# Optimization experiments

Hardware: AMD Instinct MI355X
Metric: run time of the kernel (lower is better)

## Reference

```python
import jax, jax.numpy as jnp
import numpy as np

N, D_IN, D_H, D_OUT, R, E, NB = 50000, 128, 128, 64, 4, 400000, 2

def _xavier(k, shape, fan_in, fan_out):
    # torch xavier_uniform with relu gain sqrt(2)
    lim = np.sqrt(2.0) * np.sqrt(6.0 / (fan_in + fan_out))
    return jax.random.uniform(k, shape, jnp.float32, -lim, lim)

def setup_inputs() -> dict:
    key = jax.random.key(0)
    ks = jax.random.split(key, 9)
    x = jax.random.normal(ks[0], (N, D_IN), dtype=jnp.float32)
    src = jax.random.randint(ks[1], (R, E), 0, N, dtype=jnp.int32)
    dst = jax.random.randint(ks[2], (R, E), 0, N, dtype=jnp.int32)
    inp = {"x": x, "src": src, "dst": dst}
    dims = [(D_IN, D_H), (D_H, D_H), (D_H, D_OUT)]
    for i, (di, do) in enumerate(dims):
        inp[f"basis{i}"] = _xavier(ks[3 + 2 * i], (NB, di, do), di, do)
        inp[f"coeff{i}"] = _xavier(ks[4 + 2 * i], (R, NB), NB, R)
    return inp

def _rel_layer(h, src, dst, basis, coeff):
    """One RelGraphConvLayer: per-relation basis weight + GraphConv(norm='both'),
    summed over relations (HeteroGraphConv aggregate='sum')."""
    n = h.shape[0]
    W = jnp.einsum('rb,bio->rio', coeff, basis)  # [R, d_in, d_out] basis-decomposed weights
    out = jnp.zeros((n, W.shape[-1]), dtype=h.dtype)
    for r in range(src.shape[0]):  # fixed small set of relations
        s, d = src[r], dst[r]
        ones = jnp.ones(s.shape[0], dtype=h.dtype)
        deg_out = jnp.maximum(jax.ops.segment_sum(ones, s, num_segments=n), 1.0)
        deg_in = jnp.maximum(jax.ops.segment_sum(ones, d, num_segments=n), 1.0)
        norm_src = deg_out ** -0.5
        norm_dst = deg_in ** -0.5
        # weight applied before aggregation (d_in >= d_out path of dgl GraphConv; math identical)
        hr = (h * norm_src[:, None]) @ W[r]            # [N, d_out]
        agg = jax.ops.segment_sum(hr[s], d, num_segments=n)  # SpMM via gather + scatter-add
        out = out + agg * norm_dst[:, None]
    return out

def reference(x, src, dst, basis0, coeff0, basis1, coeff1, basis2, coeff2):
    h = jax.nn.relu(_rel_layer(x, src, dst, basis0, coeff0))
    h = jax.nn.relu(_rel_layer(h, src, dst, basis1, coeff1))
    return _rel_layer(h, src, dst, basis2, coeff2)  # final layer: no activation
```

## Files before the change

kernel.cpp:

```cpp
#include <hip/hip_runtime.h>
#include <hip/hip_bf16.h>
#include <cstdint>
#include <cstddef>

#define NN 50000
#define RR 4
#define EE 400000
#define TE (RR*EE)
#define HR 25000
#define RN (RR*NN)
#define NSEG (NN*RR)
#define SCB2 782
#define NBK 512
#define BKSZ 98
#define CHA 4000
#define MAXSPAN 4608

using frag_ab = __attribute__((ext_vector_type(8))) short;
using frag_cd = __attribute__((ext_vector_type(4))) float;

static __device__ __forceinline__ unsigned short f2bf(float f) {
    union { float f; unsigned u; } v; v.f = f;
    unsigned r = (v.u + 0x7FFF + ((v.u >> 16) & 1)) >> 16;
    return (unsigned short)r;
}
static __device__ __forceinline__ unsigned pack2(float lo, float hi) {
    return (unsigned)f2bf(lo) | ((unsigned)f2bf(hi) << 16);
}
static __device__ __forceinline__ float blo(unsigned u) { return __uint_as_float(u << 16); }
static __device__ __forceinline__ float bhi(unsigned u) { return __uint_as_float(u & 0xFFFF0000u); }

__global__ __launch_bounds__(1024) void k_hist(const int* __restrict__ src,
                                               const int* __restrict__ dst,
                                               int* __restrict__ cnt_srcQ,
                                               int* __restrict__ cnt_dstQ) {
    __shared__ unsigned bins[HR / 2];
    int combo = blockIdx.x >> 3;
    int range = (blockIdx.x >> 2) & 1;
    int qc    = blockIdx.x & 3;
    int r = combo >> 1;
    int side = combo & 1;
    const int* arr = (side == 0 ? src : dst) + (size_t)r * EE + (size_t)qc * (EE / 4);
    int lo = range * HR;
    for (int i = threadIdx.x; i < HR / 2; i += 1024) bins[i] = 0;
    __syncthreads();
    const int4* a4 = (const int4*)arr;
    for (int i = threadIdx.x; i < EE / 16; i += 1024) {
        int4 v = a4[i];
        int t;
        t = v.x - lo; if ((unsigned)t < (unsigned)HR) atomicAdd(&bins[t >> 1], 1u << ((t & 1) * 16));
        t = v.y - lo; if ((unsigned)t < (unsigned)HR) atomicAdd(&bins[t >> 1], 1u << ((t & 1) * 16));
        t = v.z - lo; if ((unsigned)t < (unsigned)HR) atomicAdd(&bins[t >> 1], 1u << ((t & 1) * 16));
        t = v.w - lo; if ((unsigned)t < (unsigned)HR) atomicAdd(&bins[t >> 1], 1u << ((t & 1) * 16));
    }
    __syncthreads();
    int* outp = (side == 0 ? cnt_srcQ : cnt_dstQ) + (size_t)qc * RN + (size_t)r * NN + lo;
    for (int i = threadIdx.x; i < HR / 2; i += 1024) {
        unsigned b = bins[i];
        outp[2 * i]     = (int)(b & 0xFFFFu);
        outp[2 * i + 1] = (int)(b >> 16);
    }
}

__global__ __launch_bounds__(256) void k_sum_norms(const int* __restrict__ cnt_srcQ,
                                                   const int* __restrict__ cnt_dstQ,
                                                   float* __restrict__ nsrc,
                                                   float* __restrict__ ndst,
                                                   int* __restrict__ cntd2) {
    int i = blockIdx.x * 256 + threadIdx.x;
    if (i >= RN) return;
    int ss = cnt_srcQ[i] + cnt_srcQ[RN + i] + cnt_srcQ[2 * RN + i] + cnt_srcQ[3 * RN + i];
    int ds = cnt_dstQ[i] + cnt_dstQ[RN + i] + cnt_dstQ[2 * RN + i] + cnt_dstQ[3 * RN + i];
    nsrc[i] = 1.0f / sqrtf(fmaxf((float)ss, 1.0f));
    ndst[i] = 1.0f / sqrtf(fmaxf((float)ds, 1.0f));
    int r = i / NN, d = i - r * NN;
    cntd2[d * 4 + r] = ds;
}

__global__ __launch_bounds__(256) void k_partial(const int* __restrict__ cntd2,
                                                 int* __restrict__ part) {
    __shared__ int s[256];
    int t = threadIdx.x;
    int f = blockIdx.x * 256 + t;
    int v = (f < NSEG) ? cntd2[f] : 0;
    s[t] = v;
    __syncthreads();
    for (int off = 128; off > 0; off >>= 1) {
        if (t < off) s[t] += s[t + off];
        __syncthreads();
    }
    if (t == 0) part[blockIdx.x] = s[0];
}

__global__ __launch_bounds__(1024) void k_scan_small(const int* __restrict__ part,
                                                     int* __restrict__ offs) {
    __shared__ int s[1024];
    int t = threadIdx.x;
    s[t] = (t < SCB2) ? part[t] : 0;
    __syncthreads();
    for (int off = 1; off < 1024; off <<= 1) {
        int v = (t >= off) ? s[t - off] : 0;
        __syncthreads();
        s[t] += v;
        __syncthreads();
    }
    if (t < SCB2) offs[t] = (t == 0) ? 0 : s[t - 1];
}

__global__ __launch_bounds__(256) void k_emit(const int* __restrict__ cntd2,
                                              const int* __restrict__ offs,
                                              int* __restrict__ rp2,
                                              int* __restrict__ gcur) {
    __shared__ int s[256];
    int t = threadIdx.x;
    int f = blockIdx.x * 256 + t;
    int v = (f < NSEG) ? cntd2[f] : 0;
    s[t] = v;
    __syncthreads();
    for (int off = 1; off < 256; off <<= 1) {
        int u = (t >= off) ? s[t - off] : 0;
        __syncthreads();
        s[t] += u;
        __syncthreads();
    }
    if (f < NSEG) {
        int rv = offs[blockIdx.x] + s[t] - v;
        rp2[f] = rv;
        if (f % (BKSZ * 4) == 0) gcur[f / (BKSZ * 4)] = rv;
    }
    if (f == NSEG - 1) {
        rp2[NSEG] = TE;
        gcur[NBK - 1] = TE;
    }
}

__global__ __launch_bounds__(256) void k_fillA(const int* __restrict__ src,
                                               const int* __restrict__ dst,
                                               int* __restrict__ gcur,
                                               unsigned* __restrict__ stage) {
    __shared__ int cnt[NBK];
    __shared__ int rcur[NBK];
    int r = blockIdx.y;
    int base_e = blockIdx.x * CHA;
    int t = threadIdx.x;
    for (int i = t; i < NBK; i += 256) cnt[i] = 0;
    __syncthreads();
    const int* dr = dst + (size_t)r * EE;
    const int* sr = src + (size_t)r * EE;
    for (int i = base_e + t; i < base_e + CHA; i += 256) {
        int d = dr[i];
        atomicAdd(&cnt[d / BKSZ], 1);
    }
    __syncthreads();
    for (int i = t; i < NBK; i += 256) rcur[i] = atomicAdd(&gcur[i], cnt[i]);
    __syncthreads();
    for (int i = base_e + t; i < base_e + CHA; i += 256) {
        int d = dr[i];
        int s = sr[i];
        int b = d / BKSZ;
        int dl = d - b * BKSZ;
        int pos = atomicAdd(&rcur[b], 1);
        stage[pos] = (unsigned)s | ((unsigned)r << 16) | ((unsigned)dl << 18);
    }
}

__global__ __launch_bounds__(256) void k_fillB(const unsigned* __restrict__ stage,
                                               const int* __restrict__ rp2,
                                               const float* __restrict__ nsrc,
                                               const float* __restrict__ ndst,
                                               uint2* __restrict__ ed) {
    __shared__ unsigned imgU[MAXSPAN];
    __shared__ float imgW[MAXSPAN];
    __shared__ int lcur[BKSZ * 4];
    __shared__ float ndL[BKSZ * 4];
    int b = blockIdx.x;
    int t = threadIdx.x;
    int node0 = b * BKSZ;
    if (node0 >= NN) return;
    int nodes = min(BKSZ, NN - node0);
    int nseg_local = nodes * 4;
    int segbase = node0 * 4;
    for (int i = t; i < nseg_local; i += 256) {
        lcur[i] = rp2[segbase + i];
        ndL[i] = ndst[(i & 3) * NN + node0 + (i >> 2)];
    }
    __syncthreads();
    int S0 = rp2[segbase];
    int S1 = rp2[segbase + nseg_local];
    int span = S1 - S0;
    if (span <= MAXSPAN) {
        for (int i = S0 + t; i < S1; i += 256) {
            unsigned w = stage[i];
            int s = (int)(w & 0xFFFFu);
            int r = (int)((w >> 16) & 3u);
            int dl = (int)(w >> 18);
            int seg = dl * 4 + r;
            int pos = atomicAdd(&lcur[seg], 1);
            int idx = pos - S0;
            imgU[idx] = w & 0x3FFFFu;
            imgW[idx] = nsrc[r * NN + s] * ndL[seg];
        }
        __syncthreads();
        for (int i = t; i < span; i += 256)
            ed[S0 + i] = make_uint2(imgU[i], __float_as_uint(imgW[i]));
    } else {
        for (int i = S0 + t; i < S1; i += 256) {
            unsigned w = stage[i];
            int s = (int)(w & 0xFFFFu);
            int r = (int)((w >> 16) & 3u);
            int dl = (int)(w >> 18);
            int seg = dl * 4 + r;
            int pos = atomicAdd(&lcur[seg], 1);
            ed[pos] = make_uint2(w & 0x3FFFFu,
                                 __float_as_uint(nsrc[r * NN + s] * ndL[seg]));
        }
    }
}

__global__ __launch_bounds__(256) void k_cvt_all(const float4* __restrict__ x4,
                                                 uint2* __restrict__ o,
                                                 const float* __restrict__ B0,
                                                 const float* __restrict__ B1,
                                                 const float* __restrict__ B2,
                                                 unsigned short* __restrict__ Bt0,
                                                 unsigned short* __restrict__ Bt1,
                                                 unsigned short* __restrict__ Bt2) {
    int b = blockIdx.x;
    if (b < 6250) {
        int i = b * 256 + threadIdx.x;
        float4 v = x4[i];
        o[i] = make_uint2(pack2(v.x, v.y), pack2(v.z, v.w));
    } else {
        int t = (b - 6250) * 256 + threadIdx.x;
        if (t < 32768) {
            int k = t & 255, n = t >> 8;
            Bt0[t] = f2bf(B0[k * 128 + n]);
        } else if (t < 65536) {
            int i = t - 32768;
            int k = i & 255, n = i >> 8;
            Bt1[i] = f2bf(B1[k * 128 + n]);
        } else if (t < 81920) {
            int i = t - 65536;
            int k = i & 255, n = i >> 8;
            Bt2[i] = f2bf(B2[k * 64 + n]);
        }
    }
}

template <int BN, bool BF16OUT>
__global__ __launch_bounds__(512) void k_agg_gemm(const uint4* __restrict__ hb4,
                                                  const int* __restrict__ rp2,
                                                  const uint2* __restrict__ ed,
                                                  const float* __restrict__ coeff,
                                                  const unsigned short* __restrict__ Bt,
                                                  void* __restrict__ Cout) {
    __shared__ uint4 ldsA4[32 * 32];
    char* ldsB = (char*)ldsA4;

    int w = threadIdx.x >> 6;
    int lane = threadIdx.x & 63;
    int q = lane >> 4, hl = lane & 15;
    int node0 = blockIdx.x * 32;

    float c00 = coeff[0], c01 = coeff[1], c10 = coeff[2], c11 = coeff[3];
    float c20 = coeff[4], c21 = coeff[5], c30 = coeff[6], c31 = coeff[7];

#pragma unroll 1
    for (int k4 = 0; k4 < 4; k4++) {
        int rowl = w + k4 * 8;
        int node = node0 + rowl;
        if (node < NN) {
            float a00 = 0.f, a01 = 0.f, a02 = 0.f, a03 = 0.f;
            float a04 = 0.f, a05 = 0.f, a06 = 0.f, a07 = 0.f;
            float a10 = 0.f, a11 = 0.f, a12 = 0.f, a13 = 0.f;
            float a14 = 0.f, a15 = 0.f, a16 = 0.f, a17 = 0.f;

            int e0 = rp2[node * 4], e1 = rp2[node * 4 + 4];
            int e = e0;
            uint2 wA = make_uint2(0u, 0u), wB = make_uint2(0u, 0u);
            if (e + 7 < e1) { wA = ed[e + q]; wB = ed[e + 4 + q]; }
            for (; e + 7 < e1; e += 8) {
                uint4 hA = hb4[(size_t)(wA.x & 0xFFFFu) * 16 + hl];
                uint4 hB = hb4[(size_t)(wB.x & 0xFFFFu) * 16 + hl];
                int eN = (e + 15 < e1) ? (e + 8) : e0;
                uint2 nA = ed[eN + q];
                uint2 nB = ed[eN + 4 + q];

                int rA = (int)(wA.x >> 16);
                int rB = (int)(wB.x >> 16);
                float wsA = __uint_as_float(wA.y);
                float wsB = __uint_as_float(wB.y);
                float wa0 = (rA == 0 ? c00 : rA == 1 ? c10 : rA == 2 ? c20 : c30) * wsA;
                float wa1 = (rA == 0 ? c01 : rA == 1 ? c11 : rA == 2 ? c21 : c31) * wsA;
                float wb0 = (rB == 0 ? c00 : rB == 1 ? c10 : rB == 2 ? c20 : c30) * wsB;
                float wb1 = (rB == 0 ? c01 : rB == 1 ? c11 : rB == 2 ? c21 : c31) * wsB;

                float h0 = blo(hA.x), h1 = bhi(hA.x), h2 = blo(hA.y), h3 = bhi(hA.y);
                float h4 = blo(hA.z), h5 = bhi(hA.z), h6 = blo(hA.w), h7 = bhi(hA.w);
                a00 += wa0 * h0; a01 += wa0 * h1; a02 += wa0 * h2; a03 += wa0 * h3;
                a04 += wa0 * h4; a05 += wa0 * h5; a06 += wa0 * h6; a07 += wa0 * h7;
                a10 += wa1 * h0; a11 += wa1 * h1; a12 += wa1 * h2; a13 += wa1 * h3;
                a14 += wa1 * h4; a15 += wa1 * h5; a16 += wa1 * h6; a17 += wa1 * h7;

                h0 = blo(hB.x); h1 = bhi(hB.x); h2 = blo(hB.y); h3 = bhi(hB.y);
                h4 = blo(hB.z); h5 = bhi(hB.z); h6 = blo(hB.w); h7 = bhi(hB.w);
                a00 += wb0 * h0; a01 += wb0 * h1; a02 += wb0 * h2; a03 += wb0 * h3;
                a04 += wb0 * h4; a05 += wb0 * h5; a06 += wb0 * h6; a07 += wb0 * h7;
                a10 += wb1 * h0; a11 += wb1 * h1; a12 += wb1 * h2; a13 += wb1 * h3;
                a14 += wb1 * h4; a15 += wb1 * h5; a16 += wb1 * h6; a17 += wb1 * h7;

                wA = nA; wB = nB;
            }
            for (; e < e1; e += 4) {
                int E = e + q;
                bool act = E < e1;
                uint2 weA = ed[act ? E : e0];
                uint4 hA = hb4[(size_t)(weA.x & 0xFFFFu) * 16 + hl];
                int rA = (int)(weA.x >> 16);
                float wsA = act ? __uint_as_float(weA.y) : 0.f;
                float wa0 = (rA == 0 ? c00 : rA == 1 ? c10 : rA == 2 ? c20 : c30) * wsA;
                float wa1 = (rA == 0 ? c01 : rA == 1 ? c11 : rA == 2 ? c21 : c31) * wsA;
                float h0 = blo(hA.x), h1 = bhi(hA.x), h2 = blo(hA.y), h3 = bhi(hA.y);
                float h4 = blo(hA.z), h5 = bhi(hA.z), h6 = blo(hA.w), h7 = bhi(hA.w);
                a00 += wa0 * h0; a01 += wa0 * h1; a02 += wa0 * h2; a03 += wa0 * h3;
                a04 += wa0 * h4; a05 += wa0 * h5; a06 += wa0 * h6; a07 += wa0 * h7;
                a10 += wa1 * h0; a11 += wa1 * h1; a12 += wa1 * h2; a13 += wa1 * h3;
                a14 += wa1 * h4; a15 += wa1 * h5; a16 += wa1 * h6; a17 += wa1 * h7;
            }

            a00 += __shfl_xor(a00, 16, 64); a00 += __shfl_xor(a00, 32, 64);
            a01 += __shfl_xor(a01, 16, 64); a01 += __shfl_xor(a01, 32, 64);
            a02 += __shfl_xor(a02, 16, 64); a02 += __shfl_xor(a02, 32, 64);
            a03 += __shfl_xor(a03, 16, 64); a03 += __shfl_xor(a03, 32, 64);
            a04 += __shfl_xor(a04, 16, 64); a04 += __shfl_xor(a04, 32, 64);
            a05 += __shfl_xor(a05, 16, 64); a05 += __shfl_xor(a05, 32, 64);
            a06 += __shfl_xor(a06, 16, 64); a06 += __shfl_xor(a06, 32, 64);
            a07 += __shfl_xor(a07, 16, 64); a07 += __shfl_xor(a07, 32, 64);
            a10 += __shfl_xor(a10, 16, 64); a10 += __shfl_xor(a10, 32, 64);
            a11 += __shfl_xor(a11, 16, 64); a11 += __shfl_xor(a11, 32, 64);
            a12 += __shfl_xor(a12, 16, 64); a12 += __shfl_xor(a12, 32, 64);
            a13 += __shfl_xor(a13, 16, 64); a13 += __shfl_xor(a13, 32, 64);
            a14 += __shfl_xor(a14, 16, 64); a14 += __shfl_xor(a14, 32, 64);
            a15 += __shfl_xor(a15, 16, 64); a15 += __shfl_xor(a15, 32, 64);
            a16 += __shfl_xor(a16, 16, 64); a16 += __shfl_xor(a16, 32, 64);
            a17 += __shfl_xor(a17, 16, 64); a17 += __shfl_xor(a17, 32, 64);

            int c = q >> 1, h4 = q & 1;
            float v0 = c ? (h4 ? a14 : a10) : (h4 ? a04 : a00);
            float v1 = c ? (h4 ? a15 : a11) : (h4 ? a05 : a01);
            float v2 = c ? (h4 ? a16 : a12) : (h4 ? a06 : a02);
            float v3 = c ? (h4 ? a17 : a13) : (h4 ? a07 : a03);
            uint2 st;
            st.x = pack2(v0, v1);
            st.y = pack2(v2, v3);
            int idx8 = c * 32 + hl * 2 + h4;
            int boff = rowl * 512 + ((idx8 * 8) ^ ((rowl & 7) << 4));
            *(uint2*)(ldsB + boff) = st;
        }
    }
    __syncthreads();

    int strip = w & 1;
    int colgrp = w >> 1;
    int m = lane & 15, qq = lane >> 4;
    constexpr int NTW = BN / 64;

    frag_cd acc[NTW];
#pragma unroll
    for (int t = 0; t < NTW; t++) acc[t] = (frag_cd){0.f, 0.f, 0.f, 0.f};

    int arow = strip * 16 + m;
#pragma unroll
    for (int kc = 0; kc < 8; kc++) {
        int aoff = arow * 512 + ((qq * 16 + kc * 64) ^ ((arow & 7) << 4));
        frag_ab a = *(const frag_ab*)(ldsB + aoff);
#pragma unroll
        for (int t = 0; t < NTW; t++) {
            int ct = colgrp * NTW + t;
            frag_ab b = *(const frag_ab*)(Bt + (size_t)(ct * 16 + m) * 256 + kc * 32 + qq * 8);
            acc[t] = __builtin_amdgcn_mfma_f32_16x16x32_bf16(a, b, acc[t], 0, 0, 0);
        }
    }

    int row0 = node0 + strip * 16;
#pragma unroll
    for (int t = 0; t < NTW; t++) {
#pragma unroll
        for (int i = 0; i < 4; i++) {
            int row = row0 + qq * 4 + i;
            if (row < NN) {
                int col = (colgrp * NTW + t) * 16 + m;
                float v = acc[t][i];
                if (BF16OUT) {
                    v = fmaxf(v, 0.f);
                    ((unsigned short*)Cout)[(size_t)row * BN + col] = f2bf(v);
                } else {
                    ((float*)Cout)[(size_t)row * BN + col] = v;
                }
            }
        }
    }
}


extern "C" void kernel_launch(void* const* d_in, const int* in_sizes, int n_in,
                              void* d_out, int out_size, void* d_ws, size_t ws_size,
                              hipStream_t stream) {
    const float* x      = (const float*)d_in[0];
    const int*   src    = (const int*)d_in[1];
    const int*   dst    = (const int*)d_in[2];
    const float* basis0 = (const float*)d_in[3];
    const float* coeff0 = (const float*)d_in[4];
    const float* basis1 = (const float*)d_in[5];
    const float* coeff1 = (const float*)d_in[6];
    const float* basis2 = (const float*)d_in[7];
    const float* coeff2 = (const float*)d_in[8];
    float* out = (float*)d_out;

    char* p = (char*)d_ws;
    auto alloc = [&](size_t bytes) {
        char* r = p;
        p += (bytes + 255) & ~(size_t)255;
        return r;
    };
    int*   cnt_srcQ = (int*)alloc((size_t)4 * RN * 4);
    int*   cnt_dstQ = (int*)alloc((size_t)4 * RN * 4);
    float* nsrc     = (float*)alloc((size_t)RN * 4);
    float* ndst     = (float*)alloc((size_t)RN * 4);
    int*   cntd2    = (int*)alloc((size_t)NSEG * 4);
    int*   rp2      = (int*)alloc((size_t)(NSEG + 1) * 4);
    int*   part     = (int*)alloc((size_t)SCB2 * 4);
    int*   offs     = (int*)alloc((size_t)SCB2 * 4);
    int*   gcur     = (int*)alloc((size_t)NBK * 4);
    unsigned* stage = (unsigned*)alloc((size_t)TE * 4);
    uint2* ed       = (uint2*)alloc((size_t)TE * 8);
    unsigned* Hb    = (unsigned*)alloc((size_t)NN * 64 * 4);
    unsigned* Hb2   = (unsigned*)alloc((size_t)NN * 64 * 4);
    unsigned* Xb    = (unsigned*)alloc((size_t)NN * 64 * 4);
    unsigned short* Bt0 = (unsigned short*)alloc((size_t)128 * 256 * 2);
    unsigned short* Bt1 = (unsigned short*)alloc((size_t)128 * 256 * 2);
    unsigned short* Bt2 = (unsigned short*)alloc((size_t)64 * 256 * 2);

    k_cvt_all<<<6570, 256, 0, stream>>>((const float4*)x, (uint2*)Xb,
                                        basis0, basis1, basis2, Bt0, Bt1, Bt2);
    k_hist<<<64, 1024, 0, stream>>>(src, dst, cnt_srcQ, cnt_dstQ);
    k_sum_norms<<<(RN + 255) / 256, 256, 0, stream>>>(cnt_srcQ, cnt_dstQ, nsrc, ndst, cntd2);
    k_partial<<<SCB2, 256, 0, stream>>>(cntd2, part);
    k_scan_small<<<1, 1024, 0, stream>>>(part, offs);
    k_emit<<<SCB2, 256, 0, stream>>>(cntd2, offs, rp2, gcur);
    k_fillA<<<dim3(EE / CHA, RR), 256, 0, stream>>>(src, dst, gcur, stage);
    k_fillB<<<NBK, 256, 0, stream>>>(stage, rp2, nsrc, ndst, ed);

    int fusedBlocks = (NN + 31) / 32;

    k_agg_gemm<128, true><<<fusedBlocks, 512, 0, stream>>>(
        (const uint4*)Xb, rp2, ed, coeff0, Bt0, Hb);
    k_agg_gemm<128, true><<<fusedBlocks, 512, 0, stream>>>(
        (const uint4*)Hb, rp2, ed, coeff1, Bt1, Hb2);
    k_agg_gemm<64, false><<<fusedBlocks, 512, 0, stream>>>(
        (const uint4*)Hb2, rp2, ed, coeff2, Bt2, out);
}
```

Baseline: 378.3 us.

## Fuse preprocessing kernels and shrink aggregation-GEMM blocks to 16 nodes

Merges the histogram and bf16 conversion kernels into one launch. Folds the degree-norm computation into the block-partial reduction and replaces the separate single-block scan with a per-block prefix recompute inside the emit kernel, cutting the preprocessing chain from six launches to three. The fused aggregation+GEMM kernel now uses 256-thread blocks covering 16 nodes with no bounds checks, because 50000 divides evenly by 16; this is meant to raise occupancy and load balance. The cost is that emit redundantly sums up to 782 partials per block.

After: 376.9 us. About the same (-0.4%).

```diff
diff --git a/kernel.cpp b/kernel.cpp
--- a/kernel.cpp
+++ b/kernel.cpp
@@ -30,93 +30,120 @@
 static __device__ __forceinline__ float blo(unsigned u) { return __uint_as_float(u << 16); }
 static __device__ __forceinline__ float bhi(unsigned u) { return __uint_as_float(u & 0xFFFF0000u); }
 
-__global__ __launch_bounds__(1024) void k_hist(const int* __restrict__ src,
-                                               const int* __restrict__ dst,
-                                               int* __restrict__ cnt_srcQ,
-                                               int* __restrict__ cnt_dstQ) {
+__global__ __launch_bounds__(1024) void k_pre(const int* __restrict__ src,
+                                              const int* __restrict__ dst,
+                                              int* __restrict__ cnt_srcQ,
+                                              int* __restrict__ cnt_dstQ,
+                                              const float4* __restrict__ x4,
+                                              uint2* __restrict__ o,
+                                              const float* __restrict__ B0,
+                                              const float* __restrict__ B1,
+                                              const float* __restrict__ B2,
+                                              unsigned short* __restrict__ Bt0,
+                                              unsigned short* __restrict__ Bt1,
+                                              unsigned short* __restrict__ Bt2) {
     __shared__ unsigned bins[HR / 2];
-    int combo = blockIdx.x >> 3;
-    int range = (blockIdx.x >> 2) & 1;
-    int qc    = blockIdx.x & 3;
-    int r = combo >> 1;
-    int side = combo & 1;
-    const int* arr = (side == 0 ? src : dst) + (size_t)r * EE + (size_t)qc * (EE / 4);
-    int lo = range * HR;
-    for (int i = threadIdx.x; i < HR / 2; i += 1024) bins[i] = 0;
-    __syncthreads();
-    const int4* a4 = (const int4*)arr;
-    for (int i = threadIdx.x; i < EE / 16; i += 1024) {
-        int4 v = a4[i];
-        int t;
-        t = v.x - lo; if ((unsigned)t < (unsigned)HR) atomicAdd(&bins[t >> 1], 1u << ((t & 1) * 16));
-        t = v.y - lo; if ((unsigned)t < (unsigned)HR) atomicAdd(&bins[t >> 1], 1u << ((t & 1) * 16));
-        t = v.z - lo; if ((unsigned)t < (unsigned)HR) atomicAdd(&bins[t >> 1], 1u << ((t & 1) * 16));
-        t = v.w - lo; if ((unsigned)t < (unsigned)HR) atomicAdd(&bins[t >> 1], 1u << ((t & 1) * 16));
-    }
-    __syncthreads();
-    int* outp = (side == 0 ? cnt_srcQ : cnt_dstQ) + (size_t)qc * RN + (size_t)r * NN + lo;
-    for (int i = threadIdx.x; i < HR / 2; i += 1024) {
-        unsigned b = bins[i];
-        outp[2 * i]     = (int)(b & 0xFFFFu);
-        outp[2 * i + 1] = (int)(b >> 16);
-    }
-}
-
-__global__ __launch_bounds__(256) void k_sum_norms(const int* __restrict__ cnt_srcQ,
-                                                   const int* __restrict__ cnt_dstQ,
-                                                   float* __restrict__ nsrc,
-                                                   float* __restrict__ ndst,
-                                                   int* __restrict__ cntd2) {
-    int i = blockIdx.x * 256 + threadIdx.x;
-    if (i >= RN) return;
-    int ss = cnt_srcQ[i] + cnt_srcQ[RN + i] + cnt_srcQ[2 * RN + i] + cnt_srcQ[3 * RN + i];
-    int ds = cnt_dstQ[i] + cnt_dstQ[RN + i] + cnt_dstQ[2 * RN + i] + cnt_dstQ[3 * RN + i];
-    nsrc[i] = 1.0f / sqrtf(fmaxf((float)ss, 1.0f));
-    ndst[i] = 1.0f / sqrtf(fmaxf((float)ds, 1.0f));
-    int r = i / NN, d = i - r * NN;
-    cntd2[d * 4 + r] = ds;
-}
-
-__global__ __launch_bounds__(256) void k_partial(const int* __restrict__ cntd2,
-                                                 int* __restrict__ part) {
+    int bid = blockIdx.x;
+    if (bid < 64) {
+        int combo = bid >> 3;
+        int range = (bid >> 2) & 1;
+        int qc    = bid & 3;
+        int r = combo >> 1;
+        int side = combo & 1;
+        const int* arr = (side == 0 ? src : dst) + (size_t)r * EE + (size_t)qc * (EE / 4);
+        int lo = range * HR;
+        for (int i = threadIdx.x; i < HR / 2; i += 1024) bins[i] = 0;
+        __syncthreads();
+        const int4* a4 = (const int4*)arr;
+        for (int i = threadIdx.x; i < EE / 16; i += 1024) {
+            int4 v = a4[i];
+            int t;
+            t = v.x - lo; if ((unsigned)t < (unsigned)HR) atomicAdd(&bins[t >> 1], 1u << ((t & 1) * 16));
+            t = v.y - lo; if ((unsigned)t < (unsigned)HR) atomicAdd(&bins[t >> 1], 1u << ((t & 1) * 16));
+            t = v.z - lo; if ((unsigned)t < (unsigned)HR) atomicAdd(&bins[t >> 1], 1u << ((t & 1) * 16));
+            t = v.w - lo; if ((unsigned)t < (unsigned)HR) atomicAdd(&bins[t >> 1], 1u << ((t & 1) * 16));
+        }
+        __syncthreads();
+        int* outp = (side == 0 ? cnt_srcQ : cnt_dstQ) + (size_t)qc * RN + (size_t)r * NN + lo;
+        for (int i = threadIdx.x; i < HR / 2; i += 1024) {
+            unsigned b = bins[i];
+            outp[2 * i]     = (int)(b & 0xFFFFu);
+            outp[2 * i + 1] = (int)(b >> 16);
+        }
+    } else if (bid < 1627) {
+        int i = (bid - 64) * 1024 + threadIdx.x;
+        if (i < NN * 32) {
+            float4 v = x4[i];
+            o[i] = make_uint2(pack2(v.x, v.y), pack2(v.z, v.w));
+        }
+    } else {
+        int t = (bid - 1627) * 1024 + threadIdx.x;
+        if (t < 32768) {
+            int k = t & 255, n = t >> 8;
+            Bt0[t] = f2bf(B0[k * 128 + n]);
+        } else if (t < 65536) {
+            int i = t - 32768;
+            int k = i & 255, n = i >> 8;
+            Bt1[i] = f2bf(B1[k * 128 + n]);
+        } else {
+            int i = t - 65536;
+            int k = i & 255, n = i >> 8;
+            Bt2[i] = f2bf(B2[k * 64 + n]);
+        }
+    }
+}
+
+__global__ __launch_bounds__(256) void k_norms_partial(const int* __restrict__ cnt_srcQ,
+                                                       const int* __restrict__ cnt_dstQ,
+                                                       float* __restrict__ nsrc,
+                                                       float* __restrict__ ndst,
+                                                       int* __restrict__ cntd2,
+                                                       int* __restrict__ part) {
     __shared__ int s[256];
     int t = threadIdx.x;
     int f = blockIdx.x * 256 + t;
+    int v = 0;
+    if (f < NSEG) {
+        int d = f >> 2, r = f & 3;
+        int i = r * NN + d;
+        int ss = cnt_srcQ[i] + cnt_srcQ[RN + i] + cnt_srcQ[2 * RN + i] + cnt_srcQ[3 * RN + i];
+        int ds = cnt_dstQ[i] + cnt_dstQ[RN + i] + cnt_dstQ[2 * RN + i] + cnt_dstQ[3 * RN + i];
+        nsrc[i] = 1.0f / sqrtf(fmaxf((float)ss, 1.0f));
+        ndst[i] = 1.0f / sqrtf(fmaxf((float)ds, 1.0f));
+        cntd2[f] = ds;
+        v = ds;
+    }
+    s[t] = v;
+    __syncthreads();
+    for (int off = 128; off > 0; off >>= 1) {
+        if (t < off) s[t] += s[t + off];
+        __syncthreads();
+    }
+    if (t == 0) part[blockIdx.x] = s[0];
+}
+
+__global__ __launch_bounds__(256) void k_emit2(const int* __restrict__ cntd2,
+                                               const int* __restrict__ part,
+                                               int* __restrict__ rp2,
+                                               int* __restrict__ gcur) {
+    __shared__ int red[256];
+    __shared__ int s[256];
+    int t = threadIdx.x;
+    int bid = blockIdx.x;
+    int acc = 0;
+    for (int j = t; j < bid; j += 256) acc += part[j];
+    red[t] = acc;
+    __syncthreads();
+    for (int off = 128; off > 0; off >>= 1) {
+        if (t < off) red[t] += red[t + off];
+        __syncthreads();
+    }
+    int offs0 = red[0];
+    __syncthreads();
+    int f = bid * 256 + t;
     int v = (f < NSEG) ? cntd2[f] : 0;
     s[t] = v;
     __syncthreads();
-    for (int off = 128; off > 0; off >>= 1) {
-        if (t < off) s[t] += s[t + off];
-        __syncthreads();
-    }
-    if (t == 0) part[blockIdx.x] = s[0];
-}
-
-__global__ __launch_bounds__(1024) void k_scan_small(const int* __restrict__ part,
-                                                     int* __restrict__ offs) {
-    __shared__ int s[1024];
-    int t = threadIdx.x;
-    s[t] = (t < SCB2) ? part[t] : 0;
-    __syncthreads();
-    for (int off = 1; off < 1024; off <<= 1) {
-        int v = (t >= off) ? s[t - off] : 0;
-        __syncthreads();
-        s[t] += v;
-        __syncthreads();
-    }
-    if (t < SCB2) offs[t] = (t == 0) ? 0 : s[t - 1];
-}
-
-__global__ __launch_bounds__(256) void k_emit(const int* __restrict__ cntd2,
-                                              const int* __restrict__ offs,
-                                              int* __restrict__ rp2,
-                                              int* __restrict__ gcur) {
-    __shared__ int s[256];
-    int t = threadIdx.x;
-    int f = blockIdx.x * 256 + t;
-    int v = (f < NSEG) ? cntd2[f] : 0;
-    s[t] = v;
-    __syncthreads();
     for (int off = 1; off < 256; off <<= 1) {
         int u = (t >= off) ? s[t - off] : 0;
         __syncthreads();
@@ -124,7 +151,7 @@
         __syncthreads();
     }
     if (f < NSEG) {
-        int rv = offs[blockIdx.x] + s[t] - v;
+        int rv = offs0 + s[t] - v;
         rp2[f] = rv;
         if (f % (BKSZ * 4) == 0) gcur[f / (BKSZ * 4)] = rv;
     }
@@ -217,59 +244,29 @@
     }
 }
 
-__global__ __launch_bounds__(256) void k_cvt_all(const float4* __restrict__ x4,
-                                                 uint2* __restrict__ o,
-                                                 const float* __restrict__ B0,
-                                                 const float* __restrict__ B1,
-                                                 const float* __restrict__ B2,
-                                                 unsigned short* __restrict__ Bt0,
-                                                 unsigned short* __restrict__ Bt1,
-                                                 unsigned short* __restrict__ Bt2) {
-    int b = blockIdx.x;
-    if (b < 6250) {
-        int i = b * 256 + threadIdx.x;
-        float4 v = x4[i];
-        o[i] = make_uint2(pack2(v.x, v.y), pack2(v.z, v.w));
-    } else {
-        int t = (b - 6250) * 256 + threadIdx.x;
-        if (t < 32768) {
-            int k = t & 255, n = t >> 8;
-            Bt0[t] = f2bf(B0[k * 128 + n]);
-        } else if (t < 65536) {
-            int i = t - 32768;
-            int k = i & 255, n = i >> 8;
-            Bt1[i] = f2bf(B1[k * 128 + n]);
-        } else if (t < 81920) {
-            int i = t - 65536;
-            int k = i & 255, n = i >> 8;
-            Bt2[i] = f2bf(B2[k * 64 + n]);
-        }
-    }
-}
-
 template <int BN, bool BF16OUT>
-__global__ __launch_bounds__(512) void k_agg_gemm(const uint4* __restrict__ hb4,
+__global__ __launch_bounds__(256) void k_agg_gemm(const uint4* __restrict__ hb4,
                                                   const int* __restrict__ rp2,
                                                   const uint2* __restrict__ ed,
                                                   const float* __restrict__ coeff,
                                                   const unsigned short* __restrict__ Bt,
                                                   void* __restrict__ Cout) {
-    __shared__ uint4 ldsA4[32 * 32];
+    __shared__ uint4 ldsA4[16 * 32];
     char* ldsB = (char*)ldsA4;
 
     int w = threadIdx.x >> 6;
     int lane = threadIdx.x & 63;
     int q = lane >> 4, hl = lane & 15;
-    int node0 = blockIdx.x * 32;
+    int node0 = blockIdx.x * 16;
 
     float c00 = coeff[0], c01 = coeff[1], c10 = coeff[2], c11 = coeff[3];
     float c20 = coeff[4], c21 = coeff[5], c30 = coeff[6], c31 = coeff[7];
 
 #pragma unroll 1
     for (int k4 = 0; k4 < 4; k4++) {
-        int rowl = w + k4 * 8;
+        int rowl = w + k4 * 4;
         int node = node0 + rowl;
-        if (node < NN) {
+        {
             float a00 = 0.f, a01 = 0.f, a02 = 0.f, a03 = 0.f;
             float a04 = 0.f, a05 = 0.f, a06 = 0.f, a07 = 0.f;
             float a10 = 0.f, a11 = 0.f, a12 = 0.f, a13 = 0.f;
@@ -360,8 +357,6 @@
     }
     __syncthreads();
 
-    int strip = w & 1;
-    int colgrp = w >> 1;
     int m = lane & 15, qq = lane >> 4;
     constexpr int NTW = BN / 64;
 
@@ -369,34 +364,31 @@
 #pragma unroll
     for (int t = 0; t < NTW; t++) acc[t] = (frag_cd){0.f, 0.f, 0.f, 0.f};
 
-    int arow = strip * 16 + m;
+    int arow = m;
 #pragma unroll
     for (int kc = 0; kc < 8; kc++) {
         int aoff = arow * 512 + ((qq * 16 + kc * 64) ^ ((arow & 7) << 4));
         frag_ab a = *(const frag_ab*)(ldsB + aoff);
 #pragma unroll
         for (int t = 0; t < NTW; t++) {
-            int ct = colgrp * NTW + t;
+            int ct = w * NTW + t;
             frag_ab b = *(const frag_ab*)(Bt + (size_t)(ct * 16 + m) * 256 + kc * 32 + qq * 8);
             acc[t] = __builtin_amdgcn_mfma_f32_16x16x32_bf16(a, b, acc[t], 0, 0, 0);
         }
     }
 
-    int row0 = node0 + strip * 16;
 #pragma unroll
     for (int t = 0; t < NTW; t++) {
 #pragma unroll
         for (int i = 0; i < 4; i++) {
-            int row = row0 + qq * 4 + i;
-            if (row < NN) {
-                int col = (colgrp * NTW + t) * 16 + m;
-                float v = acc[t][i];
-                if (BF16OUT) {
-                    v = fmaxf(v, 0.f);
-                    ((unsigned short*)Cout)[(size_t)row * BN + col] = f2bf(v);
-                } else {
-                    ((float*)Cout)[(size_t)row * BN + col] = v;
-                }
+            int row = node0 + qq * 4 + i;
+            int col = (w * NTW + t) * 16 + m;
+            float v = acc[t][i];
+            if (BF16OUT) {
+                v = fmaxf(v, 0.f);
+                ((unsigned short*)Cout)[(size_t)row * BN + col] = f2bf(v);
+            } else {
+                ((float*)Cout)[(size_t)row * BN + col] = v;
             }
         }
     }
@@ -430,7 +422,6 @@
     int*   cntd2    = (int*)alloc((size_t)NSEG * 4);
     int*   rp2      = (int*)alloc((size_t)(NSEG + 1) * 4);
     int*   part     = (int*)alloc((size_t)SCB2 * 4);
-    int*   offs     = (int*)alloc((size_t)SCB2 * 4);
     int*   gcur     = (int*)alloc((size_t)NBK * 4);
     unsigned* stage = (unsigned*)alloc((size_t)TE * 4);
     uint2* ed       = (uint2*)alloc((size_t)TE * 8);
@@ -441,22 +432,20 @@
     unsigned short* Bt1 = (unsigned short*)alloc((size_t)128 * 256 * 2);
     unsigned short* Bt2 = (unsigned short*)alloc((size_t)64 * 256 * 2);
 
-    k_cvt_all<<<6570, 256, 0, stream>>>((const float4*)x, (uint2*)Xb,
-                                        basis0, basis1, basis2, Bt0, Bt1, Bt2);
-    k_hist<<<64, 1024, 0, stream>>>(src, dst, cnt_srcQ, cnt_dstQ);
-    k_sum_norms<<<(RN + 255) / 256, 256, 0, stream>>>(cnt_srcQ, cnt_dstQ, nsrc, ndst, cntd2);
-    k_partial<<<SCB2, 256, 0, stream>>>(cntd2, part);
-    k_scan_small<<<1, 1024, 0, stream>>>(part, offs);
-    k_emit<<<SCB2, 256, 0, stream>>>(cntd2, offs, rp2, gcur);
+    k_pre<<<1707, 1024, 0, stream>>>(src, dst, cnt_srcQ, cnt_dstQ,
+                                     (const float4*)x, (uint2*)Xb,
+                                     basis0, basis1, basis2, Bt0, Bt1, Bt2);
+    k_norms_partial<<<SCB2, 256, 0, stream>>>(cnt_srcQ, cnt_dstQ, nsrc, ndst, cntd2, part);
+    k_emit2<<<SCB2, 256, 0, stream>>>(cntd2, part, rp2, gcur);
     k_fillA<<<dim3(EE / CHA, RR), 256, 0, stream>>>(src, dst, gcur, stage);
     k_fillB<<<NBK, 256, 0, stream>>>(stage, rp2, nsrc, ndst, ed);
 
-    int fusedBlocks = (NN + 31) / 32;
-
-    k_agg_gemm<128, true><<<fusedBlocks, 512, 0, stream>>>(
+    int fusedBlocks = NN / 16;
+
+    k_agg_gemm<128, true><<<fusedBlocks, 256, 0, stream>>>(
         (const uint4*)Xb, rp2, ed, coeff0, Bt0, Hb);
-    k_agg_gemm<128, true><<<fusedBlocks, 512, 0, stream>>>(
+    k_agg_gemm<128, true><<<fusedBlocks, 256, 0, stream>>>(
         (const uint4*)Hb, rp2, ed, coeff1, Bt1, Hb2);
-    k_agg_gemm<64, false><<<fusedBlocks, 512, 0, stream>>>(
+    k_agg_gemm<64, false><<<fusedBlocks, 256, 0, stream>>>(
         (const uint4*)Hb2, rp2, ed, coeff2, Bt2, out);
 }
```
